# Optimization experiments

Measured on AMD Instinct MI355X. Metric: run time of the kernel, lower is better.

The kernel has to match this reference:

```python
import jax, jax.numpy as jnp
import numpy as np

DIM = 1024
MAXLEN = 2048
EPS = 1e-6


def rms_norm(x, w):
    rms = jnp.sqrt(jnp.mean(x * x, axis=-1, keepdims=True) + EPS)
    return x / rms * w


def setup_inputs() -> dict:
    key = jax.random.key(0)
    ks = jax.random.split(key, 12)
    d = DIM
    s = 0.02
    inp = {
        "x": jax.random.normal(ks[0], (8, 2048, d), dtype=jnp.float32),
        "attn_norm_w": jnp.ones((d,), jnp.float32),
        "mlp_norm_w": jnp.ones((d,), jnp.float32),
        "wq": jax.random.normal(ks[1], (d, d), jnp.float32) * s,
        "bq": jnp.zeros((d,), jnp.float32),
        "wk": jax.random.normal(ks[2], (d, d), jnp.float32) * s,
        "bk": jnp.zeros((d,), jnp.float32),
        "wv": jax.random.normal(ks[3], (d, d), jnp.float32) * s,
        "bv": jnp.zeros((d,), jnp.float32),
        "wo": jax.random.normal(ks[4], (d, d), jnp.float32) * s,
        "bo": jnp.zeros((d,), jnp.float32),
        "w1": jax.random.normal(ks[5], (d, 4 * d), jnp.float32) * s,
        "b1": jnp.zeros((4 * d,), jnp.float32),
        "w2": jax.random.normal(ks[6], (4 * d, d), jnp.float32) * s,
        "b2": jnp.zeros((d,), jnp.float32),
    }
    return inp


def reference(x, attn_norm_w, mlp_norm_w, wq, bq, wk, bk, wv, bv, wo, bo, w1, b1, w2, b2):
    b, t, d = x.shape
    xn = rms_norm(x, attn_norm_w)
    q = xn @ wq + bq
    k = xn @ wk + bk
    v = xn @ wv + bv
    # single-head attention over full dim, scaled by sqrt(d)
    scores = jnp.einsum("btd,bsd->bts", q, k) / jnp.sqrt(jnp.asarray(d, x.dtype))
    causal = jnp.tril(jnp.ones((t, t), dtype=bool))
    scores = jnp.where(causal, scores, jnp.asarray(-1e9, x.dtype))
    probs = jax.nn.softmax(scores, axis=-1)
    attn = jnp.einsum("bts,bsd->btd", probs, v)
    x = x + attn @ wo + bo
    h = rms_norm(x, mlp_norm_w)
    x = x + jax.nn.gelu(h @ w1 + b1, approximate=False) @ w2 + b2
    return x
```

## Files before the change

kernel.cpp:

```cpp
#include <hip/hip_runtime.h>
#include <hip/hip_bf16.h>

typedef __bf16 bf16;
typedef __bf16 bf16x8 __attribute__((ext_vector_type(8)));
typedef __bf16 bf16x4 __attribute__((ext_vector_type(4)));
typedef float  f32x4  __attribute__((ext_vector_type(4)));

#define DIM   1024
#define SEQ   2048
#define BATCH 8
#define NROWS (BATCH * SEQ)
#define HID   4096

__device__ __forceinline__ void async_ld16(const bf16* g, bf16* l) {
    __builtin_amdgcn_global_load_lds(
        (__attribute__((address_space(1))) void*)(g),
        (__attribute__((address_space(3))) void*)(l),
        16, 0, 0);
}

__device__ __forceinline__ f32x4 mfma16(bf16x8 a, bf16x8 b, f32x4 c) {
    return __builtin_amdgcn_mfma_f32_16x16x32_bf16(a, b, c, 0, 0, 0);
}

template<int OUTF32, int BIASMODE, int RESID, int GELU, int SCORE, int PV>
__global__ __launch_bounds__(512, 2) void gemm256_kernel(
    const bf16* __restrict__ A, size_t aB,
    const bf16* __restrict__ B, size_t bB,
    void* __restrict__ Cv, size_t cB,
    const float* __restrict__ bias,
    const float* __restrict__ resid,
    int M, int N, int K, float scale)
{
    __shared__ alignas(16) bf16 LA[2 * 2 * 8192];
    __shared__ alignas(16) bf16 LB[2 * 2 * 8192];

    const int gx = gridDim.x;
    int lin = blockIdx.y * gx + blockIdx.x;
    {
        const int nwg = gx * gridDim.y;
        const int q = nwg >> 3, r = nwg & 7;
        const int xcd = lin & 7, o = lin >> 3;
        lin = (xcd < r ? xcd * (q + 1) : r * (q + 1) + (xcd - r) * q) + o;
    }
    const int m0 = (lin / gx) * 256;
    const int n0 = (lin % gx) * 256;
    if (SCORE && n0 >= m0 + 256) return;

    const int z = blockIdx.z;
    A += (size_t)z * aB;
    B += (size_t)z * bB;

    const int t    = threadIdx.x;
    const int lane = t & 63;
    const int wave = t >> 6;
    const int wr   = wave >> 2;
    const int wc   = wave & 3;

    const int kEnd = PV ? (m0 + 256) : K;
    const int NT   = kEnd >> 6;

    const int srow = t >> 3;
    const int sd   = ((t & 7) ^ (srow & 7)) * 8;
    const bf16* gA = A + (size_t)(m0 + srow) * (size_t)K + sd;
    const bf16* gB = B + (size_t)(n0 + srow) * (size_t)K + sd;
    bf16* const lA = LA + wave * 512;
    bf16* const lB = LB + wave * 512;
    const size_t rowblk = (size_t)64 * (size_t)K;

#define STG_A(db, hf, T) do {                                               \
    const bf16* g_ = gA + (size_t)((hf) * 2) * rowblk + (size_t)(T) * 64;   \
    async_ld16(g_,          lA + ((db) * 2 + (hf)) * 8192);                 \
    async_ld16(g_ + rowblk, lA + ((db) * 2 + (hf)) * 8192 + 4096);          \
} while (0)
#define STG_B(db, hf, T) do {                                               \
    const bf16* g_ = gB + (size_t)((hf) * 2) * rowblk + (size_t)(T) * 64;   \
    async_ld16(g_,          lB + ((db) * 2 + (hf)) * 8192);                 \
    async_ld16(g_ + rowblk, lB + ((db) * 2 + (hf)) * 8192 + 4096);          \
} while (0)

    const int fr    = lane & 15;
    const int fg    = lane >> 4;
    const int pc0   = ((fg)     ^ (fr & 7)) * 8;
    const int pc1   = ((4 + fg) ^ (fr & 7)) * 8;
    const int raOff = (wr * 64 + fr) * 64;
    const int rbOff = (wc * 32 + fr) * 64;

    f32x4  acc[2][2][4][2] = {};
    bf16x8 af[4][2];
    bf16x8 bg[2][2][2];

#define LDF_A(db, hf) do { _Pragma("unroll")                                  \
    for (int mi_ = 0; mi_ < 4; ++mi_) {                                       \
        const bf16* p_ = LA + ((db) * 2 + (hf)) * 8192 + raOff + mi_ * 1024;  \
        af[mi_][0] = *(const bf16x8*)(p_ + pc0);                              \
        af[mi_][1] = *(const bf16x8*)(p_ + pc1); } } while (0)
#define LDF_B(db, hf) do { _Pragma("unroll")                                  \
    for (int ni_ = 0; ni_ < 2; ++ni_) {                                       \
        const bf16* p_ = LB + ((db) * 2 + (hf)) * 8192 + rbOff + ni_ * 1024;  \
        bg[hf][ni_][0] = *(const bf16x8*)(p_ + pc0);                          \
        bg[hf][ni_][1] = *(const bf16x8*)(p_ + pc1); } } while (0)
#define MFMAQ(qm, qn) do {                                                    \
    __builtin_amdgcn_s_setprio(1);                                            \
    _Pragma("unroll") for (int mi_ = 0; mi_ < 4; ++mi_)                       \
    _Pragma("unroll") for (int ni_ = 0; ni_ < 2; ++ni_) {                     \
        acc[qm][qn][mi_][ni_] = mfma16(af[mi_][0], bg[qn][ni_][0], acc[qm][qn][mi_][ni_]); \
        acc[qm][qn][mi_][ni_] = mfma16(af[mi_][1], bg[qn][ni_][1], acc[qm][qn][mi_][ni_]); } \
    __builtin_amdgcn_s_setprio(0);                                            \
} while (0)
#define LGKM0 do { asm volatile("s_waitcnt lgkmcnt(0)" ::: "memory");         \
                   __builtin_amdgcn_sched_barrier(0); } while (0)
#define VM2   asm volatile("s_waitcnt vmcnt(2)" ::: "memory")
#define VM4   asm volatile("s_waitcnt vmcnt(4)" ::: "memory")
#define BAR   __builtin_amdgcn_s_barrier()

    STG_A(0, 0, 0); STG_B(0, 0, 0); STG_B(0, 1, 0); STG_A(0, 1, 0);
    asm volatile("s_waitcnt vmcnt(0)" ::: "memory");
    BAR;
    LDF_A(0, 0); LDF_B(0, 0); LDF_B(0, 1);
    STG_B(1, 1, 1); STG_A(1, 0, 1);

    for (int kt = 0; kt < NT; kt += 2) {
        const int Tp1 = kt + 1;
        const int Tp2 = (kt + 2 < NT) ? kt + 2 : NT - 1;
        const int Tp3 = (kt + 3 < NT) ? kt + 3 : NT - 1;

        LGKM0;
        STG_B(1, 0, Tp1); STG_A(1, 1, Tp1);
        MFMAQ(0, 0); MFMAQ(0, 1);
        LDF_A(0, 1);
        VM2; BAR;

        LGKM0;
        STG_B(0, 1, Tp2); STG_A(0, 0, Tp2);
        MFMAQ(1, 0);
        LDF_B(1, 0);
        MFMAQ(1, 1);
        LDF_B(1, 1);
        LDF_A(1, 0);
        VM4; BAR;

        LGKM0;
        STG_B(0, 0, Tp2); STG_A(0, 1, Tp2);
        MFMAQ(0, 0); MFMAQ(0, 1);
        LDF_A(1, 1);
        VM2; BAR;

        LGKM0;
        STG_B(1, 1, Tp3); STG_A(1, 0, Tp3);
        MFMAQ(1, 0);
        LDF_B(0, 0);
        MFMAQ(1, 1);
        LDF_B(0, 1);
        LDF_A(0, 0);
        VM4; BAR;
    }

    const int col  = lane & 15;
    const int row4 = (lane >> 4) * 4;
    const size_t cOff = (size_t)z * cB;
    #pragma unroll
    for (int qm = 0; qm < 2; ++qm)
    #pragma unroll
    for (int mi = 0; mi < 4; ++mi) {
        const int mBase = m0 + qm * 128 + wr * 64 + mi * 16 + row4;
        #pragma unroll
        for (int qn = 0; qn < 2; ++qn)
        #pragma unroll
        for (int ni = 0; ni < 2; ++ni) {
            const int n = n0 + qn * 128 + wc * 32 + ni * 16 + col;
            const float bcol = (BIASMODE == 1) ? bias[n] : 0.0f;
            #pragma unroll
            for (int r = 0; r < 4; ++r) {
                const int m = mBase + r;
                float v = acc[qm][qn][mi][ni][r];
                if (BIASMODE == 1) v += bcol;
                if (BIASMODE == 2) v += bias[m];
                if (SCORE) { v *= scale; if (n > m) v = -1e30f; }
                if (GELU)  { v = 0.5f * v * (1.0f + erff(v * 0.70710678118654752f)); }
                const size_t idx = cOff + (size_t)m * (size_t)N + (size_t)n;
                if (RESID) v += resid[idx];
                if (OUTF32) ((float*)Cv)[idx] = v;
                else        ((bf16*)Cv)[idx]  = (bf16)v;
            }
        }
    }
#undef STG_A
#undef STG_B
#undef LDF_A
#undef LDF_B
#undef MFMAQ
#undef LGKM0
#undef VM2
#undef VM4
#undef BAR
}

__global__ __launch_bounds__(256) void rmsnorm_kernel(
    const float* __restrict__ x, const float* __restrict__ w, bf16* __restrict__ out)
{
    const int row = blockIdx.x;
    const int t   = threadIdx.x;
    const float4 v = ((const float4*)(x + (size_t)row * DIM))[t];
    float ss = v.x * v.x + v.y * v.y + v.z * v.z + v.w * v.w;
    #pragma unroll
    for (int off = 32; off; off >>= 1) ss += __shfl_down(ss, off);
    __shared__ float part[4];
    if ((t & 63) == 0) part[t >> 6] = ss;
    __syncthreads();
    const float tot  = part[0] + part[1] + part[2] + part[3];
    const float rinv = rsqrtf(tot * (1.0f / DIM) + 1e-6f);
    const float4 wv = ((const float4*)w)[t];
    bf16x4 o;
    o[0] = (bf16)(v.x * rinv * wv.x);
    o[1] = (bf16)(v.y * rinv * wv.y);
    o[2] = (bf16)(v.z * rinv * wv.z);
    o[3] = (bf16)(v.w * rinv * wv.w);
    *(bf16x4*)(out + (size_t)row * DIM + t * 4) = o;
}

__global__ __launch_bounds__(256) void transpose_w_kernel(
    const float* __restrict__ src, bf16* __restrict__ dst, int R, int C)
{
    __shared__ float tile[32][33];
    const int tx = threadIdx.x & 31;
    const int ty = threadIdx.x >> 5;
    const int c0 = blockIdx.x * 32;
    const int r0 = blockIdx.y * 32;
    #pragma unroll
    for (int j = 0; j < 32; j += 8)
        tile[ty + j][tx] = src[(size_t)(r0 + ty + j) * C + c0 + tx];
    __syncthreads();
    #pragma unroll
    for (int j = 0; j < 32; j += 8)
        dst[(size_t)(c0 + ty + j) * R + r0 + tx] = (bf16)tile[tx][ty + j];
}

__global__ __launch_bounds__(256) void softmax_kernel(bf16* __restrict__ S)
{
    const int t = blockIdx.x;
    const int b = blockIdx.y;
    bf16* p = S + ((size_t)b * SEQ + t) * SEQ;
    const int send = ((t >> 8) + 1) << 8;
    const int tid  = threadIdx.x;
    const int lane = tid & 63;
    const int wave = tid >> 6;

    float v[8];
    int cnt = 0;
    float m = -3.0e38f;
    for (int i = tid; i < send; i += 256) { const float f = (float)p[i]; v[cnt++] = f; m = fmaxf(m, f); }
    #pragma unroll
    for (int off = 32; off; off >>= 1) m = fmaxf(m, __shfl_down(m, off));
    __shared__ float red[4];
    if (lane == 0) red[wave] = m;
    __syncthreads();
    m = fmaxf(fmaxf(red[0], red[1]), fmaxf(red[2], red[3]));
    __syncthreads();

    float s = 0.0f;
    for (int k2 = 0; k2 < cnt; ++k2) { v[k2] = __expf(v[k2] - m); s += v[k2]; }
    #pragma unroll
    for (int off = 32; off; off >>= 1) s += __shfl_down(s, off);
    if (lane == 0) red[wave] = s;
    __syncthreads();
    s = red[0] + red[1] + red[2] + red[3];
    const float inv = 1.0f / s;
    cnt = 0;
    for (int i = tid; i < send; i += 256) p[i] = (bf16)(v[cnt++] * inv);
}

extern "C" void kernel_launch(void* const* d_in, const int* in_sizes, int n_in,
                              void* d_out, int out_size, void* d_ws, size_t ws_size,
                              hipStream_t stream)
{
    const float* x   = (const float*)d_in[0];
    const float* anw = (const float*)d_in[1];
    const float* mnw = (const float*)d_in[2];
    const float* wq  = (const float*)d_in[3];
    const float* bq  = (const float*)d_in[4];
    const float* wk  = (const float*)d_in[5];
    const float* bk  = (const float*)d_in[6];
    const float* wv  = (const float*)d_in[7];
    const float* bv  = (const float*)d_in[8];
    const float* wo  = (const float*)d_in[9];
    const float* bo  = (const float*)d_in[10];
    const float* w1  = (const float*)d_in[11];
    const float* b1  = (const float*)d_in[12];
    const float* w2  = (const float*)d_in[13];
    const float* b2  = (const float*)d_in[14];
    float* out = (float*)d_out;

    char* ws = (char*)d_ws;
    const size_t MB = 1024 * 1024;
    bf16* wqT = (bf16*)(ws + 0 * MB);
    bf16* wkT = (bf16*)(ws + 2 * MB);
    bf16* wvT = (bf16*)(ws + 4 * MB);
    bf16* woT = (bf16*)(ws + 6 * MB);
    bf16* w1T = (bf16*)(ws + 8 * MB);
    bf16* w2T = (bf16*)(ws + 16 * MB);
    bf16* xn  = (bf16*)(ws + 24 * MB);
    bf16* q   = (bf16*)(ws + 56 * MB);
    bf16* k   = (bf16*)(ws + 88 * MB);
    bf16* vT  = (bf16*)(ws + 120 * MB);
    bf16* S   = (bf16*)(ws + 152 * MB);
    bf16* attn = xn;
    bf16* h    = q;
    bf16* mid  = k;

    const dim3 blk(256);
    const dim3 blkG(512);

    transpose_w_kernel<<<dim3(DIM / 32, DIM / 32), blk, 0, stream>>>(wq, wqT, DIM, DIM);
    transpose_w_kernel<<<dim3(DIM / 32, DIM / 32), blk, 0, stream>>>(wk, wkT, DIM, DIM);
    transpose_w_kernel<<<dim3(DIM / 32, DIM / 32), blk, 0, stream>>>(wv, wvT, DIM, DIM);
    transpose_w_kernel<<<dim3(DIM / 32, DIM / 32), blk, 0, stream>>>(wo, woT, DIM, DIM);
    transpose_w_kernel<<<dim3(HID / 32, DIM / 32), blk, 0, stream>>>(w1, w1T, DIM, HID);
    transpose_w_kernel<<<dim3(DIM / 32, HID / 32), blk, 0, stream>>>(w2, w2T, HID, DIM);

    rmsnorm_kernel<<<NROWS, blk, 0, stream>>>(x, anw, xn);

    gemm256_kernel<0, 1, 0, 0, 0, 0><<<dim3(DIM / 256, NROWS / 256, 1), blkG, 0, stream>>>(
        xn, 0, wqT, 0, q, 0, bq, nullptr, NROWS, DIM, DIM, 1.0f);
    gemm256_kernel<0, 1, 0, 0, 0, 0><<<dim3(DIM / 256, NROWS / 256, 1), blkG, 0, stream>>>(
        xn, 0, wkT, 0, k, 0, bk, nullptr, NROWS, DIM, DIM, 1.0f);
    gemm256_kernel<0, 2, 0, 0, 0, 0><<<dim3(SEQ / 256, DIM / 256, BATCH), blkG, 0, stream>>>(
        wvT, 0, xn, (size_t)SEQ * DIM, vT, (size_t)DIM * SEQ, bv, nullptr, DIM, SEQ, DIM, 1.0f);

    gemm256_kernel<0, 0, 0, 0, 1, 0><<<dim3(SEQ / 256, SEQ / 256, BATCH), blkG, 0, stream>>>(
        q, (size_t)SEQ * DIM, k, (size_t)SEQ * DIM, S, (size_t)SEQ * SEQ,
        nullptr, nullptr, SEQ, SEQ, DIM, 0.03125f);

    softmax_kernel<<<dim3(SEQ, BATCH), blk, 0, stream>>>(S);

    gemm256_kernel<0, 0, 0, 0, 0, 1><<<dim3(DIM / 256, SEQ / 256, BATCH), blkG, 0, stream>>>(
        S, (size_t)SEQ * SEQ, vT, (size_t)DIM * SEQ, attn, (size_t)SEQ * DIM,
        nullptr, nullptr, SEQ, DIM, SEQ, 1.0f);

    gemm256_kernel<1, 1, 1, 0, 0, 0><<<dim3(DIM / 256, NROWS / 256, 1), blkG, 0, stream>>>(
        attn, 0, woT, 0, out, 0, bo, x, NROWS, DIM, DIM, 1.0f);

    rmsnorm_kernel<<<NROWS, blk, 0, stream>>>(out, mnw, h);

    gemm256_kernel<0, 1, 0, 1, 0, 0><<<dim3(HID / 256, NROWS / 256, 1), blkG, 0, stream>>>(
        h, 0, w1T, 0, mid, 0, b1, nullptr, NROWS, HID, DIM, 1.0f);

    gemm256_kernel<1, 1, 1, 0, 0, 0><<<dim3(DIM / 256, NROWS / 256, 1), blkG, 0, stream>>>(
        mid, 0, w2T, 0, out, 0, b2, out, NROWS, DIM, HID, 1.0f);
}
```

Baseline: 870.6 us.

## Remap wave tiles to contiguous quadrants and reschedule GEMM pipeline with ping-pong barriers

```diff
diff --git a/kernel.cpp b/kernel.cpp
--- a/kernel.cpp
+++ b/kernel.cpp
@@ -54,8 +54,8 @@
     const int t    = threadIdx.x;
     const int lane = t & 63;
     const int wave = t >> 6;
-    const int wr   = wave >> 2;
-    const int wc   = wave & 3;
+    const int wm   = wave >> 2;
+    const int wn   = wave & 3;
 
     const int kEnd = PV ? (m0 + 256) : K;
     const int NT   = kEnd >> 6;
@@ -83,23 +83,23 @@
     const int fg    = lane >> 4;
     const int pc0   = ((fg)     ^ (fr & 7)) * 8;
     const int pc1   = ((4 + fg) ^ (fr & 7)) * 8;
-    const int raOff = (wr * 64 + fr) * 64;
-    const int rbOff = (wc * 32 + fr) * 64;
+    const int raOff = wm * 8192 + fr * 64;
+    const int rbOff = (wn >> 1) * 8192 + ((wn & 1) * 64 + fr) * 64;
 
     f32x4  acc[2][2][4][2] = {};
     bf16x8 af[4][2];
     bf16x8 bg[2][2][2];
 
-#define LDF_A(db, hf) do { _Pragma("unroll")                                  \
+#define LDF_A(db, qm) do { _Pragma("unroll")                                  \
     for (int mi_ = 0; mi_ < 4; ++mi_) {                                       \
-        const bf16* p_ = LA + ((db) * 2 + (hf)) * 8192 + raOff + mi_ * 1024;  \
+        const bf16* p_ = LA + (db) * 16384 + raOff + ((qm) * 64 + mi_ * 16) * 64; \
         af[mi_][0] = *(const bf16x8*)(p_ + pc0);                              \
         af[mi_][1] = *(const bf16x8*)(p_ + pc1); } } while (0)
-#define LDF_B(db, hf) do { _Pragma("unroll")                                  \
+#define LDF_B(db, qn) do { _Pragma("unroll")                                  \
     for (int ni_ = 0; ni_ < 2; ++ni_) {                                       \
-        const bf16* p_ = LB + ((db) * 2 + (hf)) * 8192 + rbOff + ni_ * 1024;  \
-        bg[hf][ni_][0] = *(const bf16x8*)(p_ + pc0);                          \
-        bg[hf][ni_][1] = *(const bf16x8*)(p_ + pc1); } } while (0)
+        const bf16* p_ = LB + (db) * 16384 + rbOff + ((qn) * 32 + ni_ * 16) * 64; \
+        bg[qn][ni_][0] = *(const bf16x8*)(p_ + pc0);                          \
+        bg[qn][ni_][1] = *(const bf16x8*)(p_ + pc1); } } while (0)
 #define MFMAQ(qm, qn) do {                                                    \
     __builtin_amdgcn_s_setprio(1);                                            \
     _Pragma("unroll") for (int mi_ = 0; mi_ < 4; ++mi_)                       \
@@ -110,50 +110,40 @@
 } while (0)
 #define LGKM0 do { asm volatile("s_waitcnt lgkmcnt(0)" ::: "memory");         \
                    __builtin_amdgcn_sched_barrier(0); } while (0)
-#define VM2   asm volatile("s_waitcnt vmcnt(2)" ::: "memory")
+#define LGKH  asm volatile("s_waitcnt lgkmcnt(8)" ::: "memory")
 #define VM4   asm volatile("s_waitcnt vmcnt(4)" ::: "memory")
 #define BAR   __builtin_amdgcn_s_barrier()
 
-    STG_A(0, 0, 0); STG_B(0, 0, 0); STG_B(0, 1, 0); STG_A(0, 1, 0);
-    asm volatile("s_waitcnt vmcnt(0)" ::: "memory");
+    STG_A(0, 0, 0); STG_A(0, 1, 0); STG_B(0, 0, 0); STG_B(0, 1, 0);
+    STG_B(1, 0, 1); STG_B(1, 1, 1);
+    VM4;
     BAR;
-    LDF_A(0, 0); LDF_B(0, 0); LDF_B(0, 1);
-    STG_B(1, 1, 1); STG_A(1, 0, 1);
 
     for (int kt = 0; kt < NT; kt += 2) {
-        const int Tp1 = kt + 1;
         const int Tp2 = (kt + 2 < NT) ? kt + 2 : NT - 1;
         const int Tp3 = (kt + 3 < NT) ? kt + 3 : NT - 1;
 
-        LGKM0;
-        STG_B(1, 0, Tp1); STG_A(1, 1, Tp1);
-        MFMAQ(0, 0); MFMAQ(0, 1);
+        LDF_A(0, 0); LDF_B(0, 0);
+        STG_A(1, 0, kt + 1); STG_A(1, 1, kt + 1);
+        LGKH; BAR; LGKM0; MFMAQ(0, 0); BAR;
+        LDF_B(0, 1);
+        BAR; LGKM0; MFMAQ(0, 1); BAR;
         LDF_A(0, 1);
-        VM2; BAR;
-
-        LGKM0;
-        STG_B(0, 1, Tp2); STG_A(0, 0, Tp2);
-        MFMAQ(1, 0);
-        LDF_B(1, 0);
-        MFMAQ(1, 1);
+        STG_B(0, 0, Tp2);
+        BAR; LGKM0; MFMAQ(1, 0); BAR;
+        STG_B(0, 1, Tp2);
+        BAR; LGKM0; MFMAQ(1, 1); VM4; BAR;
+
+        LDF_A(1, 0); LDF_B(1, 0);
+        STG_A(0, 0, Tp2); STG_A(0, 1, Tp2);
+        LGKH; BAR; LGKM0; MFMAQ(0, 0); BAR;
         LDF_B(1, 1);
-        LDF_A(1, 0);
-        VM4; BAR;
-
-        LGKM0;
-        STG_B(0, 0, Tp2); STG_A(0, 1, Tp2);
-        MFMAQ(0, 0); MFMAQ(0, 1);
+        BAR; LGKM0; MFMAQ(0, 1); BAR;
         LDF_A(1, 1);
-        VM2; BAR;
-
-        LGKM0;
-        STG_B(1, 1, Tp3); STG_A(1, 0, Tp3);
-        MFMAQ(1, 0);
-        LDF_B(0, 0);
-        MFMAQ(1, 1);
-        LDF_B(0, 1);
-        LDF_A(0, 0);
-        VM4; BAR;
+        STG_B(1, 0, Tp3);
+        BAR; LGKM0; MFMAQ(1, 0); BAR;
+        STG_B(1, 1, Tp3);
+        BAR; LGKM0; MFMAQ(1, 1); VM4; BAR;
     }
 
     const int col  = lane & 15;
@@ -163,12 +153,12 @@
     for (int qm = 0; qm < 2; ++qm)
     #pragma unroll
     for (int mi = 0; mi < 4; ++mi) {
-        const int mBase = m0 + qm * 128 + wr * 64 + mi * 16 + row4;
+        const int mBase = m0 + wm * 128 + qm * 64 + mi * 16 + row4;
         #pragma unroll
         for (int qn = 0; qn < 2; ++qn)
         #pragma unroll
         for (int ni = 0; ni < 2; ++ni) {
-            const int n = n0 + qn * 128 + wc * 32 + ni * 16 + col;
+            const int n = n0 + wn * 64 + qn * 32 + ni * 16 + col;
             const float bcol = (BIASMODE == 1) ? bias[n] : 0.0f;
             #pragma unroll
             for (int r = 0; r < 4; ++r) {
@@ -191,7 +181,7 @@
 #undef LDF_B
 #undef MFMAQ
 #undef LGKM0
-#undef VM2
+#undef LGKH
 #undef VM4
 #undef BAR
 }
```

Result: no change. 876.1 us (+0.6%).
